# Optimization experiments

Hardware: AMD Instinct MI355X
Metric: run time of the kernel (lower is better)

Reference implementation:

```python
import jax, jax.numpy as jnp
import numpy as np

N_HEADS = 16
HIDDEN = 1024
HEAD_DIM = 64
BSZ = 4
SEQ = 1024
SCALE = HEAD_DIM ** -0.5


def setup_inputs() -> dict:
    key = jax.random.key(0)
    k_x, k_q, k_k, k_v, k_o = jax.random.split(key, 5)
    s = HIDDEN ** -0.5
    return {
        "x": jax.random.normal(k_x, (BSZ, SEQ, HIDDEN), dtype=jnp.float32),
        # torch nn.Linear weights: shape (out_features, in_features)
        "wq": jax.random.normal(k_q, (N_HEADS * HEAD_DIM, HIDDEN), dtype=jnp.float32) * s,
        "wk": jax.random.normal(k_k, (N_HEADS * HEAD_DIM, HIDDEN), dtype=jnp.float32) * s,
        "wv": jax.random.normal(k_v, (N_HEADS * HEAD_DIM, HIDDEN), dtype=jnp.float32) * s,
        "wo": jax.random.normal(k_o, (HIDDEN, N_HEADS * HEAD_DIM), dtype=jnp.float32) * s,
    }


def reference(x, wq, wk, wv, wo):
    bsz, seqlen, _ = x.shape
    xq = jnp.einsum("bsh,oh->bso", x, wq)  # (b, s, n_heads*head_dim)
    xk = jnp.einsum("bsh,oh->bso", x, wk)
    xv = jnp.einsum("bsh,oh->bso", x, wv)
    # Faithful to the original: raw view to (b, n_heads, s, head_dim), NO transpose
    xq = xq.reshape(bsz, N_HEADS, seqlen, HEAD_DIM)
    xk = xk.reshape(bsz, N_HEADS, seqlen, HEAD_DIM)
    xv = xv.reshape(bsz, N_HEADS, seqlen, HEAD_DIM)
    scores = jnp.einsum("bhid,bhjd->bhij", xq, xk) * SCALE
    scores = jax.nn.softmax(scores, axis=-1)
    out = jnp.einsum("bhij,bhjd->bhid", scores, xv)
    out = out.reshape(bsz, seqlen, N_HEADS * HEAD_DIM)  # raw view, faithful
    return jnp.einsum("bso,ho->bsh", out, wo)
```

## Files before the change

### kernel.cpp

```cpp
#include <hip/hip_runtime.h>
#include <hip/hip_bf16.h>

typedef __hip_bfloat16 bf16;
typedef __attribute__((ext_vector_type(8))) short short8;
typedef __attribute__((ext_vector_type(4))) short short4v;
typedef __attribute__((ext_vector_type(4))) float f32x4;


__device__ __forceinline__ short f2b(float x) {
    bf16 h = __float2bfloat16(x);
    return *reinterpret_cast<short*>(&h);
}
__device__ __forceinline__ f32x4 zero4() {
    f32x4 z; z[0] = 0.f; z[1] = 0.f; z[2] = 0.f; z[3] = 0.f; return z;
}
__device__ __forceinline__ void gl_lds16(const void* g, void* l) {
    __builtin_amdgcn_global_load_lds(
        (const __attribute__((address_space(1))) void*)g,
        (__attribute__((address_space(3))) void*)l, 16, 0, 0);
}

__global__ __launch_bounds__(256) void convert_in(const float* __restrict__ w0,
                                                  const float* __restrict__ w1,
                                                  const float* __restrict__ w2,
                                                  const float* __restrict__ w3,
                                                  const float* __restrict__ x,
                                                  bf16* __restrict__ Wb,
                                                  bf16* __restrict__ Xb) {
    const int y = blockIdx.y;
    const float* s;
    bf16* d;
    if (y < 4) {
        s = (y == 0) ? w0 : (y == 1) ? w1 : (y == 2) ? w2 : w3;
        d = Wb + (size_t)y * 1048576;
    } else {
        s = x + (size_t)(y - 4) * 1048576;
        d = Xb + (size_t)(y - 4) * 1048576;
    }
    const int i = (blockIdx.x * 256 + threadIdx.x) * 4;
    const float4 v = *(const float4*)(s + i);
    short4v o;
    o[0] = f2b(v.x); o[1] = f2b(v.y); o[2] = f2b(v.z); o[3] = f2b(v.w);
    *(short4v*)(d + i) = o;
}

__global__ __launch_bounds__(256) void gemm_qkv(const bf16* __restrict__ Xb,
                                                const bf16* __restrict__ Wb,
                                                bf16* __restrict__ QK,
                                                bf16* __restrict__ VT) {
    __shared__ __align__(16) bf16 As[128 * 32];
    __shared__ __align__(16) bf16 Bs[128 * 32];

    const int tid  = threadIdx.x;
    const int wave = tid >> 6;
    const int lane = tid & 63;
    const int z    = blockIdx.z;
    const int bm   = blockIdx.x * 128, bn = blockIdx.y * 128;
    const bf16* Bsrc = Wb + (size_t)z * 1048576;

    const int f0 = wave * 2048 + lane * 16, f1 = f0 + 1024;
    const char* gA0 = (const char*)(Xb + (size_t)(bm + (f0 >> 6)) * 1024) + (f0 & 63);
    const char* gA1 = (const char*)(Xb + (size_t)(bm + (f1 >> 6)) * 1024) + (f1 & 63);
    const char* gB0 = (const char*)(Bsrc + (size_t)(bn + (f0 >> 6)) * 1024) + (f0 & 63);
    const char* gB1 = (const char*)(Bsrc + (size_t)(bn + (f1 >> 6)) * 1024) + (f1 & 63);
    char* lA0 = (char*)As + wave * 2048;      char* lA1 = lA0 + 1024;
    char* lB0 = (char*)Bs + wave * 2048;      char* lB1 = lB0 + 1024;

    f32x4 acc[4][4];
#pragma unroll
    for (int i = 0; i < 4; i++)
#pragma unroll
        for (int j = 0; j < 4; j++) acc[i][j] = zero4();

    const int mrow = ((wave >> 1) * 64) + (lane & 15);
    const int nrow = ((wave & 1) * 64) + (lane & 15);
    const int kcol = (lane >> 4) * 8;

    for (int k0 = 0; k0 < 1024; k0 += 32) {
        __syncthreads();
        gl_lds16(gA0 + (size_t)k0 * 2, lA0);
        gl_lds16(gA1 + (size_t)k0 * 2, lA1);
        gl_lds16(gB0 + (size_t)k0 * 2, lB0);
        gl_lds16(gB1 + (size_t)k0 * 2, lB1);
        __syncthreads();
        short8 af[4], bfr[4];
#pragma unroll
        for (int i = 0; i < 4; i++)
            af[i] = *(const short8*)&As[(mrow + i * 16) * 32 + kcol];
#pragma unroll
        for (int j = 0; j < 4; j++)
            bfr[j] = *(const short8*)&Bs[(nrow + j * 16) * 32 + kcol];
#pragma unroll
        for (int i = 0; i < 4; i++)
#pragma unroll
            for (int j = 0; j < 4; j++)
                acc[i][j] = __builtin_amdgcn_mfma_f32_16x16x32_bf16(
                    af[i], bfr[j], acc[i][j], 0, 0, 0);
    }

    const int erow = bm + (wave >> 1) * 64 + (lane >> 4) * 4;
    const int ecol = bn + (wave & 1) * 64 + (lane & 15);
    if (z < 2) {
        bf16* C = QK + (size_t)z * 4194304;
#pragma unroll
        for (int i = 0; i < 4; i++)
#pragma unroll
            for (int j = 0; j < 4; j++)
#pragma unroll
                for (int r = 0; r < 4; r++)
                    C[(size_t)(erow + i * 16 + r) * 1024 + (ecol + j * 16)] =
                        __float2bfloat16(acc[i][j][r]);
    } else {
#pragma unroll
        for (int i = 0; i < 4; i++)
#pragma unroll
            for (int j = 0; j < 4; j++) {
                const int o  = ecol + j * 16;
                const int d  = o & 63;
                const int oh = o >> 6;
#pragma unroll
                for (int r = 0; r < 4; r++) {
                    const int rr = erow + i * 16 + r;
                    VT[(size_t)(rr >> 6) * 65536 + d * 1024 +
                       ((rr & 63) * 16 + oh)] = __float2bfloat16(acc[i][j][r]);
                }
            }
    }
}

__global__ __launch_bounds__(256, 4) void gemm_out(const bf16* __restrict__ A,
                                                   const bf16* __restrict__ B,
                                                   float* __restrict__ C) {
    __shared__ __align__(16) bf16 As[64 * 32];
    __shared__ __align__(16) bf16 Bs[64 * 32];

    const int tid  = threadIdx.x;
    const int wave = tid >> 6;
    const int lane = tid & 63;
    const int bm   = blockIdx.x * 64, bn = blockIdx.y * 64;

    const int fA = tid * 16;
    const char* gA = (const char*)(A + (size_t)(bm + (fA >> 6)) * 1024) + (fA & 63);
    const char* gB = (const char*)(B + (size_t)(bn + (fA >> 6)) * 1024) + (fA & 63);
    char* lA = (char*)As + fA;
    char* lB = (char*)Bs + fA;

    f32x4 acc[2][2];
#pragma unroll
    for (int i = 0; i < 2; i++)
#pragma unroll
        for (int j = 0; j < 2; j++) acc[i][j] = zero4();

    const int mrow = ((wave >> 1) * 32) + (lane & 15);
    const int nrow = ((wave & 1) * 32) + (lane & 15);
    const int kcol = (lane >> 4) * 8;

    for (int k0 = 0; k0 < 1024; k0 += 32) {
        __syncthreads();
        gl_lds16(gA + (size_t)k0 * 2, lA);
        gl_lds16(gB + (size_t)k0 * 2, lB);
        __syncthreads();
        short8 af[2], bfr[2];
#pragma unroll
        for (int i = 0; i < 2; i++)
            af[i] = *(const short8*)&As[(mrow + i * 16) * 32 + kcol];
#pragma unroll
        for (int j = 0; j < 2; j++)
            bfr[j] = *(const short8*)&Bs[(nrow + j * 16) * 32 + kcol];
#pragma unroll
        for (int i = 0; i < 2; i++)
#pragma unroll
            for (int j = 0; j < 2; j++)
                acc[i][j] = __builtin_amdgcn_mfma_f32_16x16x32_bf16(
                    af[i], bfr[j], acc[i][j], 0, 0, 0);
    }

    const int erow = bm + (wave >> 1) * 32 + (lane >> 4) * 4;
    const int ecol = bn + (wave & 1) * 32 + (lane & 15);
#pragma unroll
    for (int i = 0; i < 2; i++)
#pragma unroll
        for (int j = 0; j < 2; j++)
#pragma unroll
            for (int r = 0; r < 4; r++)
                C[(size_t)(erow + i * 16 + r) * 1024 + (ecol + j * 16)] =
                    acc[i][j][r];
}

#define PSTR 72
__global__ __launch_bounds__(256) void attn(bf16* __restrict__ QO,
                                            const bf16* __restrict__ K,
                                            const bf16* __restrict__ VT) {
    __shared__ __align__(16) bf16 Ks[2][64 * 64];
    __shared__ __align__(16) bf16 Vs[2][64 * 64];
    __shared__ __align__(16) bf16 Ps[128 * PSTR];

    const int tid  = threadIdx.x;
    const int wave = tid >> 6;
    const int lane = tid & 63;
    const int lg   = lane >> 4;
    const int li   = lane & 15;

    const int bid  = blockIdx.x;
    const int head = ((bid & 7) << 3) | ((bid >> 3) & 7);
    const int qt   = bid >> 6;
    bf16* Qh = QO + (size_t)head * 65536 + qt * 8192;
    const char* Khb  = (const char*)(K + (size_t)head * 65536);
    const char* VThb = (const char*)(VT + (size_t)head * 65536);

    short8 qf[2][2];
#pragma unroll
    for (int i = 0; i < 2; i++)
#pragma unroll
        for (int ks = 0; ks < 2; ks++)
            qf[i][ks] = *(const short8*)&Qh[(wave * 32 + i * 16 + li) * 64 +
                                            ks * 32 + lg * 8];

    f32x4 o_acc[2][4];
    float lp[2][4];
#pragma unroll
    for (int i = 0; i < 2; i++) {
#pragma unroll
        for (int j = 0; j < 4; j++) o_acc[i][j] = zero4();
#pragma unroll
        for (int r = 0; r < 4; r++) lp[i][r] = 0.f;
    }

    const int fs0 = wave * 2048 + lane * 16, fs1 = fs0 + 1024;
    char* KsB = (char*)Ks;
    char* VsB = (char*)Vs;
    const char* gV0 = VThb + (size_t)(fs0 >> 7) * 2048 + (fs0 & 127);
    const char* gV1 = VThb + (size_t)(fs1 >> 7) * 2048 + (fs1 & 127);

    gl_lds16(Khb + fs0, KsB + fs0);
    gl_lds16(Khb + fs1, KsB + fs1);
    gl_lds16(gV0, VsB + fs0);
    gl_lds16(gV1, VsB + fs1);

    for (int jt = 0; jt < 16; jt++) {
        const int p  = (jt & 1) * 8192;
        const int pn = 8192 - p;
        const int jn = (jt < 15) ? jt + 1 : 15;
        asm volatile("" ::: "memory");
        __builtin_amdgcn_s_barrier();
        gl_lds16(Khb + (size_t)jn * 8192 + fs0, KsB + pn + fs0);
        gl_lds16(Khb + (size_t)jn * 8192 + fs1, KsB + pn + fs1);
        gl_lds16(gV0 + jn * 128, VsB + pn + fs0);
        gl_lds16(gV1 + jn * 128, VsB + pn + fs1);
        asm volatile("s_waitcnt vmcnt(4)" ::: "memory");
        __builtin_amdgcn_s_barrier();
        asm volatile("" ::: "memory");

        const bf16* Kc = (const bf16*)(KsB + p);
        const bf16* Vc = (const bf16*)(VsB + p);

        f32x4 s_acc[2][4];
#pragma unroll
        for (int i = 0; i < 2; i++)
#pragma unroll
            for (int j = 0; j < 4; j++) s_acc[i][j] = zero4();
#pragma unroll
        for (int j = 0; j < 4; j++)
#pragma unroll
            for (int ks = 0; ks < 2; ks++) {
                short8 kf = *(const short8*)&Kc[(j * 16 + li) * 64 + ks * 32 + lg * 8];
#pragma unroll
                for (int i = 0; i < 2; i++)
                    s_acc[i][j] = __builtin_amdgcn_mfma_f32_16x16x32_bf16(
                        qf[i][ks], kf, s_acc[i][j], 0, 0, 0);
            }

#pragma unroll
        for (int i = 0; i < 2; i++)
#pragma unroll
            for (int r = 0; r < 4; r++) {
                const int prow = wave * 32 + i * 16 + lg * 4 + r;
                float ps = 0.f;
#pragma unroll
                for (int j = 0; j < 4; j++) {
                    const float pv = __expf(s_acc[i][j][r] * 0.125f);
                    ps += pv;
                    Ps[prow * PSTR + j * 16 + li] = __float2bfloat16(pv);
                }
                lp[i][r] += ps;
            }

#pragma unroll
        for (int ks = 0; ks < 2; ks++) {
            short8 pa[2];
#pragma unroll
            for (int i = 0; i < 2; i++)
                pa[i] = *(const short8*)&Ps[(wave * 32 + i * 16 + li) * PSTR +
                                            ks * 32 + lg * 8];
#pragma unroll
            for (int jd = 0; jd < 4; jd++) {
                short8 vf = *(const short8*)&Vc[(jd * 16 + li) * 64 + ks * 32 + lg * 8];
#pragma unroll
                for (int i = 0; i < 2; i++)
                    o_acc[i][jd] = __builtin_amdgcn_mfma_f32_16x16x32_bf16(
                        pa[i], vf, o_acc[i][jd], 0, 0, 0);
            }
        }
    }
    asm volatile("s_waitcnt vmcnt(0)" ::: "memory");

#pragma unroll
    for (int i = 0; i < 2; i++)
#pragma unroll
        for (int r = 0; r < 4; r++) {
            float l = lp[i][r];
#pragma unroll
            for (int off = 1; off < 16; off <<= 1) l += __shfl_xor(l, off, 16);
            const float inv = 1.f / l;
#pragma unroll
            for (int jd = 0; jd < 4; jd++)
                Qh[(wave * 32 + i * 16 + lg * 4 + r) * 64 + jd * 16 + li] =
                    __float2bfloat16(o_acc[i][jd][r] * inv);
        }
}

extern "C" void kernel_launch(void* const* d_in, const int* in_sizes, int n_in,
                              void* d_out, int out_size, void* d_ws, size_t ws_size,
                              hipStream_t stream) {
    const float* x  = (const float*)d_in[0];
    const float* wq = (const float*)d_in[1];
    const float* wk = (const float*)d_in[2];
    const float* wv = (const float*)d_in[3];
    const float* wo = (const float*)d_in[4];

    bf16* ws = (bf16*)d_ws;
    bf16* Wb = ws;
    bf16* QK = ws + 4194304;
    bf16* VT = ws + 12582912;
    bf16* Xb = (bf16*)d_out;

    convert_in<<<dim3(1024, 8), 256, 0, stream>>>(wq, wk, wv, wo, x, Wb, Xb);
    gemm_qkv<<<dim3(32, 8, 3), 256, 0, stream>>>(Xb, Wb, QK, VT);
    attn<<<512, 256, 0, stream>>>(QK, QK + 4194304, VT);
    gemm_out<<<dim3(64, 16), 256, 0, stream>>>(QK, Wb + 3145728, (float*)d_out);
}
```

Measured before the change: 182.5 us.

## Compute transposed S tile so each lane owns one query row, pack P stores

```diff
diff --git a/kernel.cpp b/kernel.cpp
--- a/kernel.cpp
+++ b/kernel.cpp
@@ -187,19 +187,19 @@
                     acc[i][j][r];
 }
 
-#define PSTR 72
 __global__ __launch_bounds__(256) void attn(bf16* __restrict__ QO,
                                             const bf16* __restrict__ K,
                                             const bf16* __restrict__ VT) {
     __shared__ __align__(16) bf16 Ks[2][64 * 64];
     __shared__ __align__(16) bf16 Vs[2][64 * 64];
-    __shared__ __align__(16) bf16 Ps[128 * PSTR];
+    __shared__ __align__(16) unsigned int Ps2[128 * 32];
 
     const int tid  = threadIdx.x;
     const int wave = tid >> 6;
     const int lane = tid & 63;
     const int lg   = lane >> 4;
     const int li   = lane & 15;
+    const int xsw  = (li & 7) << 2;
 
     const int bid  = blockIdx.x;
     const int head = ((bid & 7) << 3) | ((bid >> 3) & 7);
@@ -217,14 +217,18 @@
                                             ks * 32 + lg * 8];
 
     f32x4 o_acc[2][4];
-    float lp[2][4];
+    float lp2[2];
 #pragma unroll
     for (int i = 0; i < 2; i++) {
 #pragma unroll
         for (int j = 0; j < 4; j++) o_acc[i][j] = zero4();
-#pragma unroll
-        for (int r = 0; r < 4; r++) lp[i][r] = 0.f;
-    }
+        lp2[i] = 0.f;
+    }
+
+    unsigned int* pb[2];
+#pragma unroll
+    for (int i = 0; i < 2; i++)
+        pb[i] = Ps2 + (wave * 32 + i * 16 + li) * 32;
 
     const int fs0 = wave * 2048 + lane * 16, fs1 = fs0 + 1024;
     char* KsB = (char*)Ks;
@@ -254,11 +258,11 @@
         const bf16* Kc = (const bf16*)(KsB + p);
         const bf16* Vc = (const bf16*)(VsB + p);
 
-        f32x4 s_acc[2][4];
+        f32x4 s2[2][4];
 #pragma unroll
         for (int i = 0; i < 2; i++)
 #pragma unroll
-            for (int j = 0; j < 4; j++) s_acc[i][j] = zero4();
+            for (int j = 0; j < 4; j++) s2[i][j] = zero4();
 #pragma unroll
         for (int j = 0; j < 4; j++)
 #pragma unroll
@@ -266,32 +270,35 @@
                 short8 kf = *(const short8*)&Kc[(j * 16 + li) * 64 + ks * 32 + lg * 8];
 #pragma unroll
                 for (int i = 0; i < 2; i++)
-                    s_acc[i][j] = __builtin_amdgcn_mfma_f32_16x16x32_bf16(
-                        qf[i][ks], kf, s_acc[i][j], 0, 0, 0);
+                    s2[i][j] = __builtin_amdgcn_mfma_f32_16x16x32_bf16(
+                        kf, qf[i][ks], s2[i][j], 0, 0, 0);
             }
 
 #pragma unroll
-        for (int i = 0; i < 2; i++)
-#pragma unroll
-            for (int r = 0; r < 4; r++) {
-                const int prow = wave * 32 + i * 16 + lg * 4 + r;
-                float ps = 0.f;
-#pragma unroll
-                for (int j = 0; j < 4; j++) {
-                    const float pv = __expf(s_acc[i][j][r] * 0.125f);
-                    ps += pv;
-                    Ps[prow * PSTR + j * 16 + li] = __float2bfloat16(pv);
-                }
-                lp[i][r] += ps;
+        for (int i = 0; i < 2; i++) {
+            float ps = 0.f;
+#pragma unroll
+            for (int j = 0; j < 4; j++) {
+                const float p0 = __expf(s2[i][j][0] * 0.125f);
+                const float p1 = __expf(s2[i][j][1] * 0.125f);
+                const float p2 = __expf(s2[i][j][2] * 0.125f);
+                const float p3 = __expf(s2[i][j][3] * 0.125f);
+                ps += (p0 + p1) + (p2 + p3);
+                unsigned int w0, w1;
+                asm("v_cvt_pk_bf16_f32 %0, %1, %2" : "=v"(w0) : "v"(p0), "v"(p1));
+                asm("v_cvt_pk_bf16_f32 %0, %1, %2" : "=v"(w1) : "v"(p2), "v"(p3));
+                *(unsigned long long*)(pb[i] + ((j * 8 + lg * 2) ^ xsw)) =
+                    ((unsigned long long)w1 << 32) | w0;
             }
+            lp2[i] += ps;
+        }
 
 #pragma unroll
         for (int ks = 0; ks < 2; ks++) {
             short8 pa[2];
 #pragma unroll
             for (int i = 0; i < 2; i++)
-                pa[i] = *(const short8*)&Ps[(wave * 32 + i * 16 + li) * PSTR +
-                                            ks * 32 + lg * 8];
+                pa[i] = *(const short8*)(pb[i] + ((ks * 16 + lg * 4) ^ xsw));
 #pragma unroll
             for (int jd = 0; jd < 4; jd++) {
                 short8 vf = *(const short8*)&Vc[(jd * 16 + li) * 64 + ks * 32 + lg * 8];
@@ -305,18 +312,20 @@
     asm volatile("s_waitcnt vmcnt(0)" ::: "memory");
 
 #pragma unroll
-    for (int i = 0; i < 2; i++)
+    for (int i = 0; i < 2; i++) {
+        float l = lp2[i];
+        l += __shfl_xor(l, 16);
+        l += __shfl_xor(l, 32);
 #pragma unroll
         for (int r = 0; r < 4; r++) {
-            float l = lp[i][r];
-#pragma unroll
-            for (int off = 1; off < 16; off <<= 1) l += __shfl_xor(l, off, 16);
-            const float inv = 1.f / l;
+            const float lr = __shfl(l, (lane & 48) | (lg * 4 + r));
+            const float inv = 1.f / lr;
 #pragma unroll
             for (int jd = 0; jd < 4; jd++)
                 Qh[(wave * 32 + i * 16 + lg * 4 + r) * 64 + jd * 16 + li] =
                     __float2bfloat16(o_acc[i][jd][r] * inv);
         }
+    }
 }
 
 extern "C" void kernel_launch(void* const* d_in, const int* in_sizes, int n_in,
```

Result: no change. 179.7 us (-1.6%).
